# Kernel tuning notes

Measured on AMD Instinct MI355X. Metric: run time of the kernel, lower is better.

## Reference

```python
import jax, jax.numpy as jnp
import numpy as np

HEADS = 6
WSIZE = 8
SHIFTS = 4
EPS = 1e-5


def conv1x1(x, w, b=None):
    # x: (B,C,H,W), w: (O,C)
    y = jnp.einsum('bchw,oc->bohw', x, w)
    if b is not None:
        y = y + b[None, :, None, None]
    return y


def spatial_shift(x):
    # ShiftConv2d1 depthwise fixed-kernel conv == per-group spatial shift with zero pad
    C = x.shape[1]
    g = C // 5
    x0, x1, x2, x3, x4 = (x[:, :g], x[:, g:2 * g], x[:, 2 * g:3 * g],
                          x[:, 3 * g:4 * g], x[:, 4 * g:])
    left = jnp.pad(x0[:, :, :, 1:], ((0, 0), (0, 0), (0, 0), (0, 1)))   # kernel (1,2)
    right = jnp.pad(x1[:, :, :, :-1], ((0, 0), (0, 0), (0, 0), (1, 0)))  # kernel (1,0)
    up = jnp.pad(x2[:, :, 1:, :], ((0, 0), (0, 0), (0, 1), (0, 0)))      # kernel (2,1)
    down = jnp.pad(x3[:, :, :-1, :], ((0, 0), (0, 0), (1, 0), (0, 0)))   # kernel (0,1)
    return jnp.concatenate([left, right, up, down, x4], axis=1)


def window_attn(xb, ws, heads, shifts):
    # xb: (B, 2*heads*c, H, W); self-similarity attention q@q^T (no separate K, no scaling)
    if shifts > 0:
        xb = jnp.roll(xb, (-(ws // 2), -(ws // 2)), axis=(2, 3))
    b, c2, H, W = xb.shape
    cd = c2 // (2 * heads)
    nh, nw = H // ws, W // ws
    t = xb.reshape(b, 2, heads, cd, nh, ws, nw, ws)
    t = t.transpose(1, 0, 4, 6, 2, 5, 7, 3).reshape(2, b * nh * nw, heads, ws * ws, cd)
    q, v = t[0], t[1]
    atn = jax.nn.softmax(jnp.einsum('whnc,whmc->whnm', q, q), axis=-1)
    o = jnp.einsum('whnm,whmc->whnc', atn, v)
    o = o.reshape(b, nh, nw, heads, ws, ws, cd)
    o = o.transpose(0, 3, 6, 1, 4, 2, 5).reshape(b, heads * cd, H, W)
    if shifts > 0:
        o = jnp.roll(o, (ws // 2, ws // 2), axis=(2, 3))
    return o


def setup_inputs() -> dict:
    key = jax.random.key(0)
    ks = jax.random.split(key, 8)
    B, C, H, W = 2, 180, 256, 256
    s = 0.05
    return {
        'x': jax.random.normal(ks[0], (B, C, H, W), jnp.float32),
        'w0': jax.random.normal(ks[1], (2 * C, C), jnp.float32) * s,
        'b0': jnp.zeros((2 * C,), jnp.float32),
        'w1': jax.random.normal(ks[2], (C, 2 * C), jnp.float32) * s,
        'b1': jnp.zeros((C,), jnp.float32),
        'w_in': jax.random.normal(ks[3], (2 * C, C), jnp.float32) * s,
        'b_in': jnp.zeros((2 * C,), jnp.float32),
        'bn_g': jnp.ones((2 * C,), jnp.float32),
        'bn_b': jnp.zeros((2 * C,), jnp.float32),
        'w_out': jax.random.normal(ks[4], (C, C), jnp.float32) * s,
        'b_out': jnp.zeros((C,), jnp.float32),
    }


def reference(x, w0, b0, w1, b1, w_in, b_in, bn_g, bn_b, w_out, b_out):
    # --- LFE (shift-conv FFN), exp_ratio=2, relu ---
    y = conv1x1(spatial_shift(x), w0, b0)
    y = jax.nn.relu(y)
    y = conv1x1(spatial_shift(y), w1, b1)
    x = y + x
    # --- GMSA (3 parallel shifted-window self-similarity attentions) ---
    z = conv1x1(x, w_in, b_in)
    mu = z.mean(axis=(0, 2, 3), keepdims=True)
    var = z.var(axis=(0, 2, 3), keepdims=True)  # biased, matching BN training forward
    z = (z - mu) / jnp.sqrt(var + EPS) * bn_g[None, :, None, None] + bn_b[None, :, None, None]
    cs = z.shape[1] // 3
    sizes = [WSIZE // 4, WSIZE // 2, WSIZE]
    outs = [window_attn(z[:, i * cs:(i + 1) * cs], sizes[i], HEADS, SHIFTS)
            for i in range(3)]
    out = conv1x1(jnp.concatenate(outs, axis=1), w_out, b_out)
    return out + x
```

## Files before the change

kernel.cpp:

```cpp
#include <hip/hip_runtime.h>
#include <hip/hip_bf16.h>

#define HWSZ 65536
#define NPIX 131072

typedef unsigned short u16;
typedef __bf16 bf16x8 __attribute__((ext_vector_type(8)));
typedef float f32x4 __attribute__((ext_vector_type(4)));
typedef unsigned short u16x2 __attribute__((ext_vector_type(2)));
typedef unsigned short u16x4 __attribute__((ext_vector_type(4)));
typedef unsigned short u16x8 __attribute__((ext_vector_type(8)));

__device__ inline u16 f2bf(float f) {
    unsigned int x = __builtin_bit_cast(unsigned int, f);
    unsigned int r = x + 0x7FFFu + ((x >> 16) & 1u);
    return (u16)(r >> 16);
}
__device__ inline float bf2f(u16 u) {
    unsigned int x = ((unsigned int)u) << 16;
    return __builtin_bit_cast(float, x);
}

__global__ __launch_bounds__(256) void prep_w(
    const float* __restrict__ w0, const float* __restrict__ w1,
    const float* __restrict__ wi, const float* __restrict__ wo,
    u16* __restrict__ W0p, u16* __restrict__ W1p,
    u16* __restrict__ Wip, u16* __restrict__ Wop)
{
    const int i = blockIdx.x * 256 + threadIdx.x;
    {
        const int r = i / 192, c = i % 192;
        const bool ok = (r < 360) && (c < 180);
        W0p[i] = ok ? f2bf(w0[r * 180 + c]) : (u16)0;
        Wip[i] = ok ? f2bf(wi[r * 180 + c]) : (u16)0;
    }
    {
        const int r = i / 384, c = i % 384;
        W1p[i] = (r < 180 && c < 360) ? f2bf(w1[r * 360 + c]) : (u16)0;
    }
    if (i < 36864) {
        const int r = i / 192, c = i % 192;
        Wop[i] = (r < 180 && c < 180) ? f2bf(wo[r * 180 + c]) : (u16)0;
    }
}

template<int CI, int CO, int G, int INM, int XSTR, bool RELU, int RES, int OUTM, int OSTR>
__global__ __launch_bounds__(256, 4) void conv_v5(
    const void* __restrict__ Xv, const u16* __restrict__ Wp,
    const float* __restrict__ bias, const void* __restrict__ Rv,
    void* __restrict__ Yv)
{
    constexpr int CI_PAD = ((CI + 31) / 32) * 32;
    constexpr int NSTEP  = CI_PAD / 32;
    constexpr int LDK    = 40;

    __shared__ u16 Xt[2][64 * LDK];

    const int tid  = threadIdx.x;
    const int p0   = blockIdx.x * 64;
    const int b    = p0 >> 16;
    const int pix0 = p0 & 65535;
    const int h    = pix0 >> 8;
    const int w0c  = pix0 & 255;
    const int lane = tid & 63, wid = tid >> 6;
    const int lr = lane & 15, lg = lane >> 4;
    const int co_wave = blockIdx.y * 192 + wid * 48;

    const float* Xf = (const float*)Xv + (size_t)b * CI * HWSZ;
    const u16*   Xh = (const u16*)Xv;

    const int xn  = tid & 63;
    const int k4a = tid >> 6;

    auto loadX = [&](int kt, u16x4 (&r)[2]) {
        #pragma unroll
        for (int it = 0; it < 2; ++it) {
            const int k4 = k4a + it * 4;
            const int c0 = kt + k4 * 4;
            u16x4 v = {0, 0, 0, 0};
            if (c0 < CI) {
                int dh = 0, dw = 0;
                if (G > 0) {
                    const int g = c0 / G;
                    if      (g == 0) dw = 1;
                    else if (g == 1) dw = -1;
                    else if (g == 2) dh = 1;
                    else if (g == 3) dh = -1;
                }
                const int hh = h + dh;
                const int wp = w0c + xn + dw;
                if (hh >= 0 && hh < 256 && wp >= 0 && wp < 256) {
                    if constexpr (INM == 1) {
                        const size_t pg = (size_t)((b << 16) | (hh << 8) | wp);
                        v = *(const u16x4*)&Xh[pg * XSTR + c0];
                    } else {
                        const float* xs = Xf + (size_t)c0 * HWSZ + hh * 256 + wp;
                        #pragma unroll
                        for (int j = 0; j < 4; ++j) v[j] = f2bf(xs[(size_t)j * HWSZ]);
                    }
                }
            }
            r[it] = v;
        }
    };

    auto loadW = [&](int kt, bf16x8 (&a)[3]) {
        #pragma unroll
        for (int mf = 0; mf < 3; ++mf)
            a[mf] = *(const bf16x8*)&Wp[(size_t)(co_wave + mf * 16 + lr) * CI_PAD + kt + lg * 8];
    };

    auto writeLDS = [&](u16x4 (&r)[2], int buf) {
        *(u16x4*)&Xt[buf][xn * LDK + k4a * 4]       = r[0];
        *(u16x4*)&Xt[buf][xn * LDK + (k4a + 4) * 4] = r[1];
    };

    f32x4 acc[3][4] = {};
    u16x4 rawQ[2][2];
    bf16x8 af[2][3];

    loadX(0, rawQ[0]);
    loadW(0, af[0]);
    loadX(32, rawQ[1]);
    writeLDS(rawQ[0], 0);

    #pragma unroll
    for (int s = 0; s < NSTEP; ++s) {
        const int cur = s & 1, nxt = cur ^ 1;
        __syncthreads();
        if (s + 2 < NSTEP) loadX((s + 2) * 32, rawQ[cur]);
        if (s + 1 < NSTEP) loadW((s + 1) * 32, af[nxt]);
        bf16x8 bfr[4];
        #pragma unroll
        for (int nf = 0; nf < 4; ++nf)
            bfr[nf] = *(const bf16x8*)&Xt[cur][(nf * 16 + lr) * LDK + lg * 8];
        #pragma unroll
        for (int mf = 0; mf < 3; ++mf)
            #pragma unroll
            for (int nf = 0; nf < 4; ++nf)
                acc[mf][nf] = __builtin_amdgcn_mfma_f32_16x16x32_bf16(
                    af[cur][mf], bfr[nf], acc[mf][nf], 0, 0, 0);
        if (s + 1 < NSTEP) writeLDS(rawQ[nxt], nxt);
    }

    const float* Rf = (const float*)Rv;
    const u16*   Rh = (const u16*)Rv;
    #pragma unroll
    for (int mf = 0; mf < 3; ++mf) {
        const int co_b = co_wave + mf * 16 + lg * 4;
        if (co_b >= CO) continue;
        #pragma unroll
        for (int nf = 0; nf < 4; ++nf) {
            const int pl = pix0 + nf * 16 + lr;
            const size_t pg = (size_t)p0 + nf * 16 + lr;
            float v[4];
            #pragma unroll
            for (int r = 0; r < 4; ++r) {
                v[r] = acc[mf][nf][r] + bias[co_b + r];
                if (RELU) v[r] = fmaxf(v[r], 0.f);
            }
            if (RES == 1) {
                #pragma unroll
                for (int r = 0; r < 4; ++r)
                    v[r] += Rf[((size_t)(b * CO + co_b + r)) * HWSZ + pl];
            }
            if (RES == 2) {
                u16x4 rr = *(const u16x4*)&Rh[pg * 180 + co_b];
                #pragma unroll
                for (int r = 0; r < 4; ++r) v[r] += bf2f(rr[r]);
            }
            if (OUTM == 1) {
                u16x4 o;
                #pragma unroll
                for (int r = 0; r < 4; ++r) o[r] = f2bf(v[r]);
                *(u16x4*)&((u16*)Yv)[pg * OSTR + co_b] = o;
            } else {
                #pragma unroll
                for (int r = 0; r < 4; ++r)
                    ((float*)Yv)[((size_t)(b * CO + co_b + r)) * HWSZ + pl] = v[r];
            }
        }
    }
}

__global__ __launch_bounds__(256) void bn_part(const u16* __restrict__ zt,
                                               float* __restrict__ part)
{
    const int tid = threadIdx.x;
    const int oc  = tid & 63;
    const int pp  = tid >> 6;
    if (oc >= 45) return;
    const int stripe = blockIdx.x * 4 + pp;
    const int pb = blockIdx.x * 1024 + pp;
    float s[8] = {}, q[8] = {};
    for (int i = 0; i < 256; ++i) {
        const int p = pb + i * 4;
        u16x8 t = *(const u16x8*)&zt[(size_t)p * 360 + oc * 8];
        #pragma unroll
        for (int j = 0; j < 8; ++j) {
            float v = bf2f(t[j]);
            s[j] += v; q[j] += v * v;
        }
    }
    float* pr = part + ((size_t)stripe * 45 + oc) * 16;
    #pragma unroll
    for (int j = 0; j < 8; ++j) { pr[j] = s[j]; pr[8 + j] = q[j]; }
}

__global__ __launch_bounds__(256) void bn_fin(const float* __restrict__ part,
                                              const float* __restrict__ g,
                                              const float* __restrict__ bb,
                                              float* __restrict__ sc,
                                              float* __restrict__ sh)
{
    const int oc = blockIdx.x;
    const int t  = threadIdx.x;
    const float* p1 = part + ((size_t)t * 45 + oc) * 16;
    const float* p2 = part + ((size_t)(t + 256) * 45 + oc) * 16;
    float v[16];
    #pragma unroll
    for (int k = 0; k < 16; ++k) v[k] = p1[k] + p2[k];
    #pragma unroll
    for (int k = 0; k < 16; ++k)
        for (int m = 32; m; m >>= 1) v[k] += __shfl_xor(v[k], m, 64);
    __shared__ float red[4][16];
    if ((t & 63) == 0) {
        #pragma unroll
        for (int k = 0; k < 16; ++k) red[t >> 6][k] = v[k];
    }
    __syncthreads();
    if (t == 0) {
        const float invN = 1.f / (float)NPIX;
        #pragma unroll
        for (int j = 0; j < 8; ++j) {
            const int c = oc * 8 + j;
            float su = red[0][j] + red[1][j] + red[2][j] + red[3][j];
            float sq = red[0][8+j] + red[1][8+j] + red[2][8+j] + red[3][8+j];
            float mean = su * invN;
            float var  = sq * invN - mean * mean;
            float istd = 1.f / sqrtf(var + 1e-5f);
            float s = g[c] * istd;
            sc[c] = s;
            sh[c] = bb[c] - mean * s;
        }
    }
}

template<int WS>
__global__ __launch_bounds__(256) void attn_v2(
    const u16* __restrict__ zt, const float* __restrict__ scale,
    const float* __restrict__ shiftc, u16* __restrict__ ot, int chunk)
{
    constexpr int NP  = WS * WS;
    constexpr int GPB = 256 / NP;
    constexpr int SH  = WS / 2;
    constexpr int NW  = 256 / WS;

    __shared__ float qs[256 * 12];
    __shared__ float vs[256 * 12];

    const int tid = threadIdx.x;
    const int lg  = tid / NP;
    const int n   = tid % NP;
    const int gidx = blockIdx.x * GPB + lg;

    const int head = gidx % 6;
    const int win  = gidx / 6;
    const int wcol = win % NW;
    const int tmp  = win / NW;
    const int wrow = tmp % NW;
    const int b    = tmp / NW;

    const int i = n / WS, j = n % WS;
    const int hh = (wrow * WS + i + SH) & 255;
    const int ww = (wcol * WS + j + SH) & 255;
    const size_t zrow = (size_t)((b << 16) | (hh << 8) | ww) * 360;

    const int cq = chunk * 120 + head * 10;
    const int cv = cq + 60;

    float q[10];
    float* qrow = &qs[tid * 12];
    float* vrow = &vs[tid * 12];
    #pragma unroll
    for (int c2 = 0; c2 < 5; ++c2) {
        u16x2 uq = *(const u16x2*)&zt[zrow + cq + c2 * 2];
        u16x2 uv = *(const u16x2*)&zt[zrow + cv + c2 * 2];
        float q0 = bf2f(uq[0]) * scale[cq + c2 * 2]     + shiftc[cq + c2 * 2];
        float q1 = bf2f(uq[1]) * scale[cq + c2 * 2 + 1] + shiftc[cq + c2 * 2 + 1];
        float v0 = bf2f(uv[0]) * scale[cv + c2 * 2]     + shiftc[cv + c2 * 2];
        float v1 = bf2f(uv[1]) * scale[cv + c2 * 2 + 1] + shiftc[cv + c2 * 2 + 1];
        q[c2 * 2] = q0; q[c2 * 2 + 1] = q1;
        qrow[c2 * 2] = q0; qrow[c2 * 2 + 1] = q1;
        vrow[c2 * 2] = v0; vrow[c2 * 2 + 1] = v1;
    }
    qrow[10] = 0.f; qrow[11] = 0.f;
    vrow[10] = 0.f; vrow[11] = 0.f;
    __syncthreads();

    const float* qg = &qs[(lg * NP) * 12];
    const float* vg = &vs[(lg * NP) * 12];

    float mx = -1e30f;
    for (int m = 0; m < NP; ++m) {
        f32x4 a0 = *(const f32x4*)&qg[m * 12];
        f32x4 a1 = *(const f32x4*)&qg[m * 12 + 4];
        f32x4 a2 = *(const f32x4*)&qg[m * 12 + 8];
        float d = q[0]*a0[0] + q[1]*a0[1] + q[2]*a0[2] + q[3]*a0[3]
                + q[4]*a1[0] + q[5]*a1[1] + q[6]*a1[2] + q[7]*a1[3]
                + q[8]*a2[0] + q[9]*a2[1];
        mx = fmaxf(mx, d);
    }
    float s = 0.f;
    float o[10] = {};
    for (int m = 0; m < NP; ++m) {
        f32x4 a0 = *(const f32x4*)&qg[m * 12];
        f32x4 a1 = *(const f32x4*)&qg[m * 12 + 4];
        f32x4 a2 = *(const f32x4*)&qg[m * 12 + 8];
        float d = q[0]*a0[0] + q[1]*a0[1] + q[2]*a0[2] + q[3]*a0[3]
                + q[4]*a1[0] + q[5]*a1[1] + q[6]*a1[2] + q[7]*a1[3]
                + q[8]*a2[0] + q[9]*a2[1];
        float e = __expf(d - mx);
        s += e;
        f32x4 b0 = *(const f32x4*)&vg[m * 12];
        f32x4 b1 = *(const f32x4*)&vg[m * 12 + 4];
        f32x4 b2 = *(const f32x4*)&vg[m * 12 + 8];
        o[0] += e * b0[0]; o[1] += e * b0[1]; o[2] += e * b0[2]; o[3] += e * b0[3];
        o[4] += e * b1[0]; o[5] += e * b1[1]; o[6] += e * b1[2]; o[7] += e * b1[3];
        o[8] += e * b2[0]; o[9] += e * b2[1];
    }
    const float inv = 1.f / s;
    u16* orow = ot + (size_t)((b << 16) | (hh << 8) | ww) * 180 + chunk * 60 + head * 10;
    #pragma unroll
    for (int c2 = 0; c2 < 5; ++c2) {
        u16x2 ov;
        ov[0] = f2bf(o[c2 * 2] * inv);
        ov[1] = f2bf(o[c2 * 2 + 1] * inv);
        *(u16x2*)&orow[c2 * 2] = ov;
    }
}

extern "C" void kernel_launch(void* const* d_in, const int* in_sizes, int n_in,
                              void* d_out, int out_size, void* d_ws, size_t ws_size,
                              hipStream_t stream)
{
    const float* x     = (const float*)d_in[0];
    const float* w0    = (const float*)d_in[1];
    const float* b0    = (const float*)d_in[2];
    const float* w1    = (const float*)d_in[3];
    const float* b1    = (const float*)d_in[4];
    const float* w_in  = (const float*)d_in[5];
    const float* b_in  = (const float*)d_in[6];
    const float* bn_g  = (const float*)d_in[7];
    const float* bn_b  = (const float*)d_in[8];
    const float* w_out = (const float*)d_in[9];
    const float* b_out = (const float*)d_in[10];
    float* out = (float*)d_out;

    u16* y   = (u16*)d_ws;
    u16* x1b = y   + (size_t)NPIX * 360;
    u16* ot  = x1b + (size_t)NPIX * 180;
    u16* W0p = ot  + (size_t)NPIX * 180;
    u16* Wip = W0p + 384 * 192;
    u16* W1p = Wip + 384 * 192;
    u16* Wop = W1p + 192 * 384;
    float* part   = (float*)(Wop + 192 * 192);
    float* scale  = part + 512 * 45 * 16;
    float* shiftc = scale + 360;
    u16* zt = y;

    dim3 blk(256);

    prep_w<<<dim3(288), blk, 0, stream>>>(w0, w1, w_in, w_out, W0p, W1p, Wip, Wop);

    conv_v5<180, 360, 36, 0, 0,   true,  0, 1, 360>
        <<<dim3(2048, 2), blk, 0, stream>>>(x, W0p, b0, nullptr, y);
    conv_v5<360, 180, 72, 1, 360, false, 1, 1, 180>
        <<<dim3(2048, 1), blk, 0, stream>>>(y, W1p, b1, x, x1b);
    conv_v5<180, 360, 0,  1, 180, false, 0, 1, 360>
        <<<dim3(2048, 2), blk, 0, stream>>>(x1b, Wip, b_in, nullptr, zt);
    bn_part<<<dim3(128), blk, 0, stream>>>(zt, part);
    bn_fin<<<dim3(45), blk, 0, stream>>>(part, bn_g, bn_b, scale, shiftc);
    attn_v2<2><<<dim3(3072), blk, 0, stream>>>(zt, scale, shiftc, ot, 0);
    attn_v2<4><<<dim3(3072), blk, 0, stream>>>(zt, scale, shiftc, ot, 1);
    attn_v2<8><<<dim3(3072), blk, 0, stream>>>(zt, scale, shiftc, ot, 2);
    conv_v5<180, 180, 0,  1, 180, false, 2, 0, 0>
        <<<dim3(2048, 1), blk, 0, stream>>>(ot, Wop, b_out, x1b, out);
}
```

Before: 423.6 us.

## Stage full input tile into LDS once and drop per-step double buffering

Measured after the change: 457.7 us. +8.1%, slower.

```diff
diff --git a/kernel.cpp b/kernel.cpp
--- a/kernel.cpp
+++ b/kernel.cpp
@@ -44,17 +44,17 @@
     }
 }
 
-template<int CI, int CO, int G, int INM, int XSTR, bool RELU, int RES, int OUTM, int OSTR>
-__global__ __launch_bounds__(256, 4) void conv_v5(
+template<int CI, int CO, int G, int INM, bool RELU, int RES, int OUTM>
+__global__ __launch_bounds__(256, 4) void conv_v6(
     const void* __restrict__ Xv, const u16* __restrict__ Wp,
     const float* __restrict__ bias, const void* __restrict__ Rv,
     void* __restrict__ Yv)
 {
     constexpr int CI_PAD = ((CI + 31) / 32) * 32;
     constexpr int NSTEP  = CI_PAD / 32;
-    constexpr int LDK    = 40;
-
-    __shared__ u16 Xt[2][64 * LDK];
+    constexpr int XROW   = CI_PAD + 8;
+
+    __shared__ u16 Xt[64 * XROW];
 
     const int tid  = threadIdx.x;
     const int p0   = blockIdx.x * 64;
@@ -69,14 +69,13 @@
     const float* Xf = (const float*)Xv + (size_t)b * CI * HWSZ;
     const u16*   Xh = (const u16*)Xv;
 
-    const int xn  = tid & 63;
-    const int k4a = tid >> 6;
-
-    auto loadX = [&](int kt, u16x4 (&r)[2]) {
-        #pragma unroll
-        for (int it = 0; it < 2; ++it) {
-            const int k4 = k4a + it * 4;
-            const int c0 = kt + k4 * 4;
+    if constexpr (INM == 1) {
+        constexpr int CPP = CI_PAD / 4;
+        #pragma unroll
+        for (int it = 0; it < CPP / 4; ++it) {
+            const int e  = it * 256 + tid;
+            const int px = e / CPP;
+            const int c0 = (e - px * CPP) * 4;
             u16x4 v = {0, 0, 0, 0};
             if (c0 < CI) {
                 int dh = 0, dw = 0;
@@ -88,21 +87,43 @@
                     else if (g == 3) dh = -1;
                 }
                 const int hh = h + dh;
-                const int wp = w0c + xn + dw;
-                if (hh >= 0 && hh < 256 && wp >= 0 && wp < 256) {
-                    if constexpr (INM == 1) {
-                        const size_t pg = (size_t)((b << 16) | (hh << 8) | wp);
-                        v = *(const u16x4*)&Xh[pg * XSTR + c0];
-                    } else {
-                        const float* xs = Xf + (size_t)c0 * HWSZ + hh * 256 + wp;
-                        #pragma unroll
-                        for (int j = 0; j < 4; ++j) v[j] = f2bf(xs[(size_t)j * HWSZ]);
+                const int wp = w0c + px + dw;
+                if (hh >= 0 && hh < 256 && wp >= 0 && wp < 256)
+                    v = *(const u16x4*)&Xh[(size_t)((b << 16) | (hh << 8) | wp) * CI + c0];
+            }
+            *(u16x4*)&Xt[px * XROW + c0] = v;
+        }
+    } else {
+        #pragma unroll
+        for (int it = 0; it < CI_PAD / 16; ++it) {
+            const int e  = it * 256 + tid;
+            const int c  = e >> 4, pq = e & 15;
+            u16 vals[4] = {0, 0, 0, 0};
+            if (c < CI) {
+                int dh = 0, dw = 0;
+                if (G > 0) {
+                    const int g = c / G;
+                    if      (g == 0) dw = 1;
+                    else if (g == 1) dw = -1;
+                    else if (g == 2) dh = 1;
+                    else if (g == 3) dh = -1;
+                }
+                const int hh = h + dh;
+                if (hh >= 0 && hh < 256) {
+                    const float* xs = Xf + (size_t)c * HWSZ + hh * 256;
+                    #pragma unroll
+                    for (int j = 0; j < 4; ++j) {
+                        const int wp = w0c + pq * 4 + j + dw;
+                        if (wp >= 0 && wp < 256) vals[j] = f2bf(xs[wp]);
                     }
                 }
             }
-            r[it] = v;
-        }
-    };
+            #pragma unroll
+            for (int j = 0; j < 4; ++j)
+                Xt[(pq * 4 + j) * XROW + c] = vals[j];
+        }
+    }
+    __syncthreads();
 
     auto loadW = [&](int kt, bf16x8 (&a)[3]) {
         #pragma unroll
@@ -110,37 +131,23 @@
             a[mf] = *(const bf16x8*)&Wp[(size_t)(co_wave + mf * 16 + lr) * CI_PAD + kt + lg * 8];
     };
 
-    auto writeLDS = [&](u16x4 (&r)[2], int buf) {
-        *(u16x4*)&Xt[buf][xn * LDK + k4a * 4]       = r[0];
-        *(u16x4*)&Xt[buf][xn * LDK + (k4a + 4) * 4] = r[1];
-    };
-
     f32x4 acc[3][4] = {};
-    u16x4 rawQ[2][2];
     bf16x8 af[2][3];
-
-    loadX(0, rawQ[0]);
     loadW(0, af[0]);
-    loadX(32, rawQ[1]);
-    writeLDS(rawQ[0], 0);
 
     #pragma unroll
     for (int s = 0; s < NSTEP; ++s) {
-        const int cur = s & 1, nxt = cur ^ 1;
-        __syncthreads();
-        if (s + 2 < NSTEP) loadX((s + 2) * 32, rawQ[cur]);
-        if (s + 1 < NSTEP) loadW((s + 1) * 32, af[nxt]);
+        if (s + 1 < NSTEP) loadW((s + 1) * 32, af[(s + 1) & 1]);
         bf16x8 bfr[4];
         #pragma unroll
         for (int nf = 0; nf < 4; ++nf)
-            bfr[nf] = *(const bf16x8*)&Xt[cur][(nf * 16 + lr) * LDK + lg * 8];
+            bfr[nf] = *(const bf16x8*)&Xt[(nf * 16 + lr) * XROW + s * 32 + lg * 8];
         #pragma unroll
         for (int mf = 0; mf < 3; ++mf)
             #pragma unroll
             for (int nf = 0; nf < 4; ++nf)
                 acc[mf][nf] = __builtin_amdgcn_mfma_f32_16x16x32_bf16(
-                    af[cur][mf], bfr[nf], acc[mf][nf], 0, 0, 0);
-        if (s + 1 < NSTEP) writeLDS(rawQ[nxt], nxt);
+                    af[s & 1][mf], bfr[nf], acc[mf][nf], 0, 0, 0);
     }
 
     const float* Rf = (const float*)Rv;
@@ -173,7 +180,7 @@
                 u16x4 o;
                 #pragma unroll
                 for (int r = 0; r < 4; ++r) o[r] = f2bf(v[r]);
-                *(u16x4*)&((u16*)Yv)[pg * OSTR + co_b] = o;
+                *(u16x4*)&((u16*)Yv)[pg * CO + co_b] = o;
             } else {
                 #pragma unroll
                 for (int r = 0; r < 4; ++r)
@@ -373,17 +380,17 @@
 
     prep_w<<<dim3(288), blk, 0, stream>>>(w0, w1, w_in, w_out, W0p, W1p, Wip, Wop);
 
-    conv_v5<180, 360, 36, 0, 0,   true,  0, 1, 360>
+    conv_v6<180, 360, 36, 0, true,  0, 1>
         <<<dim3(2048, 2), blk, 0, stream>>>(x, W0p, b0, nullptr, y);
-    conv_v5<360, 180, 72, 1, 360, false, 1, 1, 180>
+    conv_v6<360, 180, 72, 1, false, 1, 1>
         <<<dim3(2048, 1), blk, 0, stream>>>(y, W1p, b1, x, x1b);
-    conv_v5<180, 360, 0,  1, 180, false, 0, 1, 360>
+    conv_v6<180, 360, 0,  1, false, 0, 1>
         <<<dim3(2048, 2), blk, 0, stream>>>(x1b, Wip, b_in, nullptr, zt);
     bn_part<<<dim3(128), blk, 0, stream>>>(zt, part);
     bn_fin<<<dim3(45), blk, 0, stream>>>(part, bn_g, bn_b, scale, shiftc);
     attn_v2<2><<<dim3(3072), blk, 0, stream>>>(zt, scale, shiftc, ot, 0);
     attn_v2<4><<<dim3(3072), blk, 0, stream>>>(zt, scale, shiftc, ot, 1);
     attn_v2<8><<<dim3(3072), blk, 0, stream>>>(zt, scale, shiftc, ot, 2);
-    conv_v5<180, 180, 0,  1, 180, false, 2, 0, 0>
+    conv_v6<180, 180, 0,  1, false, 2, 0>
         <<<dim3(2048, 1), blk, 0, stream>>>(ot, Wop, b_out, x1b, out);
 }
```

## Double conv pixel tile to 128 and interleave output-channel halves in block order

Applied to the files above, without the earlier changes.

New measurement: 414.4 us. 1.02x faster.

```diff
diff --git a/kernel.cpp b/kernel.cpp
--- a/kernel.cpp
+++ b/kernel.cpp
@@ -44,8 +44,8 @@
     }
 }
 
-template<int CI, int CO, int G, int INM, int XSTR, bool RELU, int RES, int OUTM, int OSTR>
-__global__ __launch_bounds__(256, 4) void conv_v5(
+template<int CI, int CO, int G, int INM, int XSTR, bool RELU, int RES, int OUTM, int OSTR, bool COSPLIT>
+__global__ __launch_bounds__(256) void conv_v8(
     const void* __restrict__ Xv, const u16* __restrict__ Wp,
     const float* __restrict__ bias, const void* __restrict__ Rv,
     void* __restrict__ Yv)
@@ -54,28 +54,36 @@
     constexpr int NSTEP  = CI_PAD / 32;
     constexpr int LDK    = 40;
 
-    __shared__ u16 Xt[2][64 * LDK];
-
-    const int tid  = threadIdx.x;
-    const int p0   = blockIdx.x * 64;
+    __shared__ u16 Xt[2][128 * LDK];
+
+    const int tid = threadIdx.x;
+    const int bid = blockIdx.x;
+    int px_tile, co0;
+    if (COSPLIT) {
+        co0     = ((bid >> 3) & 1) * 192;
+        px_tile = ((bid >> 4) << 3) | (bid & 7);
+    } else {
+        co0 = 0; px_tile = bid;
+    }
+    const int p0   = px_tile << 7;
     const int b    = p0 >> 16;
     const int pix0 = p0 & 65535;
     const int h    = pix0 >> 8;
     const int w0c  = pix0 & 255;
     const int lane = tid & 63, wid = tid >> 6;
     const int lr = lane & 15, lg = lane >> 4;
-    const int co_wave = blockIdx.y * 192 + wid * 48;
+    const int co_wave = co0 + wid * 48;
 
     const float* Xf = (const float*)Xv + (size_t)b * CI * HWSZ;
     const u16*   Xh = (const u16*)Xv;
 
-    const int xn  = tid & 63;
-    const int k4a = tid >> 6;
-
-    auto loadX = [&](int kt, u16x4 (&r)[2]) {
-        #pragma unroll
-        for (int it = 0; it < 2; ++it) {
-            const int k4 = k4a + it * 4;
+    const int xn  = tid & 127;
+    const int k4a = tid >> 7;
+
+    auto loadX = [&](int kt, u16x4 (&r)[4]) {
+        #pragma unroll
+        for (int it = 0; it < 4; ++it) {
+            const int k4 = k4a + it * 2;
             const int c0 = kt + k4 * 4;
             u16x4 v = {0, 0, 0, 0};
             if (c0 < CI) {
@@ -91,8 +99,7 @@
                 const int wp = w0c + xn + dw;
                 if (hh >= 0 && hh < 256 && wp >= 0 && wp < 256) {
                     if constexpr (INM == 1) {
-                        const size_t pg = (size_t)((b << 16) | (hh << 8) | wp);
-                        v = *(const u16x4*)&Xh[pg * XSTR + c0];
+                        v = *(const u16x4*)&Xh[(size_t)((b << 16) | (hh << 8) | wp) * XSTR + c0];
                     } else {
                         const float* xs = Xf + (size_t)c0 * HWSZ + hh * 256 + wp;
                         #pragma unroll
@@ -110,37 +117,39 @@
             a[mf] = *(const bf16x8*)&Wp[(size_t)(co_wave + mf * 16 + lr) * CI_PAD + kt + lg * 8];
     };
 
-    auto writeLDS = [&](u16x4 (&r)[2], int buf) {
-        *(u16x4*)&Xt[buf][xn * LDK + k4a * 4]       = r[0];
-        *(u16x4*)&Xt[buf][xn * LDK + (k4a + 4) * 4] = r[1];
+    auto writeLDS = [&](u16x4 (&r)[4], int buf) {
+        #pragma unroll
+        for (int it = 0; it < 4; ++it)
+            *(u16x4*)&Xt[buf][xn * LDK + (k4a + it * 2) * 4] = r[it];
     };
 
-    f32x4 acc[3][4] = {};
-    u16x4 rawQ[2][2];
+    f32x4 acc[3][8] = {};
+    u16x4 raw[2][4];
     bf16x8 af[2][3];
 
-    loadX(0, rawQ[0]);
+    loadX(0, raw[0]);
     loadW(0, af[0]);
-    loadX(32, rawQ[1]);
-    writeLDS(rawQ[0], 0);
+    writeLDS(raw[0], 0);
 
     #pragma unroll
     for (int s = 0; s < NSTEP; ++s) {
         const int cur = s & 1, nxt = cur ^ 1;
         __syncthreads();
-        if (s + 2 < NSTEP) loadX((s + 2) * 32, rawQ[cur]);
-        if (s + 1 < NSTEP) loadW((s + 1) * 32, af[nxt]);
-        bf16x8 bfr[4];
-        #pragma unroll
-        for (int nf = 0; nf < 4; ++nf)
+        if (s + 1 < NSTEP) {
+            loadX((s + 1) * 32, raw[nxt]);
+            loadW((s + 1) * 32, af[nxt]);
+        }
+        bf16x8 bfr[8];
+        #pragma unroll
+        for (int nf = 0; nf < 8; ++nf)
             bfr[nf] = *(const bf16x8*)&Xt[cur][(nf * 16 + lr) * LDK + lg * 8];
         #pragma unroll
         for (int mf = 0; mf < 3; ++mf)
             #pragma unroll
-            for (int nf = 0; nf < 4; ++nf)
+            for (int nf = 0; nf < 8; ++nf)
                 acc[mf][nf] = __builtin_amdgcn_mfma_f32_16x16x32_bf16(
                     af[cur][mf], bfr[nf], acc[mf][nf], 0, 0, 0);
-        if (s + 1 < NSTEP) writeLDS(rawQ[nxt], nxt);
+        if (s + 1 < NSTEP) writeLDS(raw[nxt], nxt);
     }
 
     const float* Rf = (const float*)Rv;
@@ -150,7 +159,7 @@
         const int co_b = co_wave + mf * 16 + lg * 4;
         if (co_b >= CO) continue;
         #pragma unroll
-        for (int nf = 0; nf < 4; ++nf) {
+        for (int nf = 0; nf < 8; ++nf) {
             const int pl = pix0 + nf * 16 + lr;
             const size_t pg = (size_t)p0 + nf * 16 + lr;
             float v[4];
@@ -373,17 +382,17 @@
 
     prep_w<<<dim3(288), blk, 0, stream>>>(w0, w1, w_in, w_out, W0p, W1p, Wip, Wop);
 
-    conv_v5<180, 360, 36, 0, 0,   true,  0, 1, 360>
-        <<<dim3(2048, 2), blk, 0, stream>>>(x, W0p, b0, nullptr, y);
-    conv_v5<360, 180, 72, 1, 360, false, 1, 1, 180>
-        <<<dim3(2048, 1), blk, 0, stream>>>(y, W1p, b1, x, x1b);
-    conv_v5<180, 360, 0,  1, 180, false, 0, 1, 360>
-        <<<dim3(2048, 2), blk, 0, stream>>>(x1b, Wip, b_in, nullptr, zt);
+    conv_v8<180, 360, 36, 0, 0,   true,  0, 1, 360, true>
+        <<<dim3(2048), blk, 0, stream>>>(x, W0p, b0, nullptr, y);
+    conv_v8<360, 180, 72, 1, 360, false, 1, 1, 180, false>
+        <<<dim3(1024), blk, 0, stream>>>(y, W1p, b1, x, x1b);
+    conv_v8<180, 360, 0,  1, 180, false, 0, 1, 360, true>
+        <<<dim3(2048), blk, 0, stream>>>(x1b, Wip, b_in, nullptr, zt);
     bn_part<<<dim3(128), blk, 0, stream>>>(zt, part);
     bn_fin<<<dim3(45), blk, 0, stream>>>(part, bn_g, bn_b, scale, shiftc);
     attn_v2<2><<<dim3(3072), blk, 0, stream>>>(zt, scale, shiftc, ot, 0);
     attn_v2<4><<<dim3(3072), blk, 0, stream>>>(zt, scale, shiftc, ot, 1);
     attn_v2<8><<<dim3(3072), blk, 0, stream>>>(zt, scale, shiftc, ot, 2);
-    conv_v5<180, 180, 0,  1, 180, false, 2, 0, 0>
-        <<<dim3(2048, 1), blk, 0, stream>>>(ot, Wop, b_out, x1b, out);
-}
+    conv_v8<180, 180, 0,  1, 180, false, 2, 0, 0, false>
+        <<<dim3(1024), blk, 0, stream>>>(ot, Wop, b_out, x1b, out);
+}
```
